# Optimization experiments

Hardware: AMD Instinct MI355X
Metric: run time of the kernel (lower is better)

The kernel has to match this reference:

```python
import jax, jax.numpy as jnp
import numpy as np

COMMITMENT_COST = 0.25
DECAY = 0.99
EPSILON = 1e-05


def setup_inputs() -> dict:
    key = jax.random.key(0)
    k1, k2, k3 = jax.random.split(key, 3)
    B, C, H, W = 64, 64, 64, 64  # C == embedding_dim
    K, D = 1024, 64
    return {
        "inputs": jax.random.normal(k1, (B, C, H, W), dtype=jnp.float32),
        "weight": jax.random.normal(k2, (K, D), dtype=jnp.float32),
        "ema_cluster_size": jnp.ones((K,), dtype=jnp.float32),
        "ema_w": jax.random.normal(k3, (K, D), dtype=jnp.float32),
    }


def reference(inputs, weight, ema_cluster_size, ema_w):
    K, D = weight.shape
    # NCHW -> NHWC, flatten to [N, D]
    x = jnp.transpose(inputs, (0, 2, 3, 1))
    flat = x.reshape(-1, D)
    # squared L2 distances to all codebook entries: [N, K]
    distances = (
        jnp.sum(flat * flat, axis=1, keepdims=True)
        + jnp.sum(weight * weight, axis=1)
        - 2.0 * flat @ weight.T
    )
    idx = jnp.argmin(distances, axis=1)  # [N]
    # training-mode EMA update (replaces the one-hot scatter + matmuls with segment sums)
    counts = jax.ops.segment_sum(jnp.ones_like(idx, dtype=flat.dtype), idx, num_segments=K)
    dw = jax.ops.segment_sum(flat, idx, num_segments=K)  # encodings.T @ flat_input
    cs = ema_cluster_size * DECAY + (1.0 - DECAY) * counts
    n = jnp.sum(cs)
    cs = (cs + EPSILON) / (n + K * EPSILON) * n  # Laplace smoothing
    ew = ema_w * DECAY + (1.0 - DECAY) * dw
    new_weight = ew / cs[:, None]
    # quantize with the UPDATED codebook (matches in-place torch order)
    quantized = new_weight[idx].reshape(x.shape)
    e_latent_loss = jnp.mean(jnp.square(jax.lax.stop_gradient(quantized) - x))
    loss = COMMITMENT_COST * e_latent_loss
    quantized_st = x + jax.lax.stop_gradient(quantized - x)  # straight-through
    return loss, jnp.transpose(quantized_st, (0, 3, 1, 2)), idx[:, None]
```

## Files before the change

kernel.cpp:

```cpp
#include <hip/hip_runtime.h>

#define K_CODES 1024
#define D_DIM   64
#define N_ROWS  262144
#define HW      4096
#define CHW     262144
#define N_ELEM  16777216
#define DECAY   0.99f
#define OMD     0.01f
#define EPS_F   1e-05f
#define MARGIN_BF 0.008f
#define FLAG_CAP 32768
#define SEG_CAP  2048
#define NHB      64
#define BROWS    128

typedef __attribute__((ext_vector_type(8))) short bf16x8;
typedef __attribute__((ext_vector_type(4))) float f32x4;

constexpr size_t OFF_LOSS    = 0;
constexpr size_t OFF_FLAGCNT = 8;
constexpr size_t OFF_DONE    = 12;
constexpr size_t ZERO_BYTES  = 64;
constexpr size_t OFF_W2F     = 64;
constexpr size_t OFF_W2D     = 4160;
constexpr size_t OFF_CS     = 12352;
constexpr size_t OFF_GOFF    = 16448;
constexpr size_t OFF_DW      = 20608;
constexpr size_t OFF_NEWW    = 282752;
constexpr size_t OFF_IDX     = 544896;
constexpr size_t OFF_HISTB   = 1593472;
constexpr size_t OFF_SORT    = 1855616;
constexpr size_t OFF_FLAGS   = 1855616;
constexpr size_t OFF_WFRAG   = 1986688;

__device__ __forceinline__ short f2bf(float f) {
    unsigned u = __float_as_uint(f);
    u += 0x7fffu + ((u >> 16) & 1u);
    return (short)(u >> 16);
}
__device__ __forceinline__ float bf2f(short h) {
    return __uint_as_float(((unsigned)(unsigned short)h) << 16);
}

__device__ __forceinline__ void gload_lds16(const float4* g, void* l) {
    __builtin_amdgcn_global_load_lds(
        (const __attribute__((address_space(1))) void*)g,
        (__attribute__((address_space(3))) void*)l, 16, 0, 0);
}

__global__ __launch_bounds__(256) void prep_kernel(
    const float* __restrict__ w, short* __restrict__ wfrag,
    float* __restrict__ w2f, double* __restrict__ w2d) {
    int t = threadIdx.x;
    if (blockIdx.x < 32) {
        int gid = blockIdx.x * 256 + t;
        int j = gid >> 7, h = (gid >> 6) & 1, L = gid & 63;
        int code = j * 16 + (L & 15);
        int kb = h * 32 + ((L >> 4) << 3);
        const float* wp = w + code * D_DIM + kb;
        short hi[8], lo[8];
#pragma unroll
        for (int i = 0; i < 8; ++i) {
            float v = wp[i];
            short hb = f2bf(v);
            hi[i] = hb;
            lo[i] = f2bf(v - bf2f(hb));
        }
        short* dh = wfrag + (size_t)(((j * 2 + h) * 2 + 0) * 64 + L) * 8;
        short* dl = wfrag + (size_t)(((j * 2 + h) * 2 + 1) * 64 + L) * 8;
#pragma unroll
        for (int i = 0; i < 8; ++i) { dh[i] = hi[i]; dl[i] = lo[i]; }
    } else {
        int k = (blockIdx.x - 32) * 256 + t;
        const float* wk = w + k * D_DIM;
        float sf = 0.f; double sd = 0.0;
#pragma unroll
        for (int d = 0; d < D_DIM; ++d) {
            float wv = wk[d];
            sf = fmaf(wv, wv, sf);
            sd = fma((double)wv, (double)wv, sd);
        }
        w2f[k] = sf; w2d[k] = sd;
    }
}

__global__ __launch_bounds__(256) __attribute__((amdgpu_waves_per_eu(2, 4)))
void argmin_kernel(
    const float* __restrict__ inp, const short* __restrict__ wfrag,
    const float* __restrict__ w2f, int* __restrict__ idx_ws,
    float* __restrict__ out_idx_f, float* __restrict__ xt,
    int* __restrict__ flagcnt, int* __restrict__ flaglist) {
    __shared__ float w2s[K_CODES];
    __shared__ alignas(16) char smem_u[64 * 68 * 4];
    __shared__ alignas(16) short bufA[8192];
    float (*xs)[68] = (float (*)[68])smem_u;
    short* bufB = (short*)smem_u;

    int t = threadIdx.x;
    ((float4*)w2s)[t] = ((const float4*)w2f)[t];

    int rowbase = blockIdx.x * BROWS;
    int b = rowbase >> 12, hwb = rowbase & (HW - 1);
    const float* xp = inp + (size_t)b * CHW + hwb;
    int lane = t & 63, wave = t >> 6;
    int q = lane >> 4, col = lane & 15;

    bf16x8 aH[2][2], aL[2][2];

    for (int p = 0; p < 2; ++p) {
#pragma unroll
        for (int it = 0; it < 16; ++it) {
            int d = wave * 16 + it;
            xs[lane][d] = xp[(size_t)d * HW + p * 64 + lane];
        }
        __syncthreads();

        float4* xt4 = (float4*)(xt + (size_t)(rowbase + p * 64) * D_DIM);
#pragma unroll
        for (int i2 = 0; i2 < 4; ++i2) {
            int c2 = t + i2 * 256;
            xt4[c2] = ((const float4*)xs[c2 >> 4])[c2 & 15];
        }

        if ((wave >> 1) == p) {
#pragma unroll
            for (int s2 = 0; s2 < 2; ++s2) {
                int rl = (wave & 1) * 32 + s2 * 16 + col;
#pragma unroll
                for (int h = 0; h < 2; ++h) {
#pragma unroll
                    for (int i = 0; i < 8; ++i) {
                        float v = xs[rl][h * 32 + q * 8 + i];
                        short hb = f2bf(v);
                        aH[s2][h][i] = hb;
                        aL[s2][h][i] = f2bf(v - bf2f(hb));
                    }
                }
            }
        }
        __syncthreads();
    }

    float best[2][4], best2[2][4];
#pragma unroll
    for (int s2 = 0; s2 < 2; ++s2)
#pragma unroll
        for (int r = 0; r < 4; ++r) { best[s2][r] = 3.4e38f; best2[s2][r] = 3.4e38f; }
    const float4* wsrc = (const float4*)wfrag;

    {
        const float4* src = wsrc + t;
        char* nb = (char*)bufA + wave * 1024;
#pragma unroll
        for (int i2 = 0; i2 < 4; ++i2)
            gload_lds16(src + i2 * 256, nb + i2 * 4096);
    }

    for (int st = 0; st < 16; ++st) {
        asm volatile("s_waitcnt vmcnt(0)" ::: "memory");
        __syncthreads();
        if (st < 15) {
            const float4* src = wsrc + (size_t)(st + 1) * 1024 + t;
            char* nb = ((st & 1) ? (char*)bufA : (char*)bufB) + wave * 1024;
#pragma unroll
            for (int i2 = 0; i2 < 4; ++i2)
                gload_lds16(src + i2 * 256, nb + i2 * 4096);
        }
        const bf16x8* wt = (const bf16x8*)((st & 1) ? bufB : bufA);

#pragma unroll
        for (int jj = 0; jj < 4; ++jj) {
            int j = st * 4 + jj;
            bf16x8 bh0 = wt[(jj * 4 + 0) * 64 + lane];
            bf16x8 bl0 = wt[(jj * 4 + 1) * 64 + lane];
            bf16x8 bh1 = wt[(jj * 4 + 2) * 64 + lane];
            bf16x8 bl1 = wt[(jj * 4 + 3) * 64 + lane];
            f32x4 acc0 = {0.f, 0.f, 0.f, 0.f};
            f32x4 acc1 = {0.f, 0.f, 0.f, 0.f};
            acc0 = __builtin_amdgcn_mfma_f32_16x16x32_bf16(aL[0][0], bh0, acc0, 0, 0, 0);
            acc1 = __builtin_amdgcn_mfma_f32_16x16x32_bf16(aL[1][0], bh0, acc1, 0, 0, 0);
            acc0 = __builtin_amdgcn_mfma_f32_16x16x32_bf16(aL[0][1], bh1, acc0, 0, 0, 0);
            acc1 = __builtin_amdgcn_mfma_f32_16x16x32_bf16(aL[1][1], bh1, acc1, 0, 0, 0);
            acc0 = __builtin_amdgcn_mfma_f32_16x16x32_bf16(aH[0][0], bl0, acc0, 0, 0, 0);
            acc1 = __builtin_amdgcn_mfma_f32_16x16x32_bf16(aH[1][0], bl0, acc1, 0, 0, 0);
            acc0 = __builtin_amdgcn_mfma_f32_16x16x32_bf16(aH[0][1], bl1, acc0, 0, 0, 0);
            acc1 = __builtin_amdgcn_mfma_f32_16x16x32_bf16(aH[1][1], bl1, acc1, 0, 0, 0);
            acc0 = __builtin_amdgcn_mfma_f32_16x16x32_bf16(aH[0][0], bh0, acc0, 0, 0, 0);
            acc1 = __builtin_amdgcn_mfma_f32_16x16x32_bf16(aH[1][0], bh0, acc1, 0, 0, 0);
            acc0 = __builtin_amdgcn_mfma_f32_16x16x32_bf16(aH[0][1], bh1, acc0, 0, 0, 0);
            acc1 = __builtin_amdgcn_mfma_f32_16x16x32_bf16(aH[1][1], bh1, acc1, 0, 0, 0);
            float w2c = w2s[j * 16 + col];
#pragma unroll
            for (int s2 = 0; s2 < 2; ++s2) {
#pragma unroll
                for (int r = 0; r < 4; ++r) {
                    float s = fmaf(-2.f, (s2 ? acc1 : acc0)[r], w2c);
                    float key = __int_as_float(
                        (__float_as_int(s) & ~63) | j);
                    best2[s2][r] = fminf(best2[s2][r], fmaxf(key, best[s2][r]));
                    best[s2][r]  = fminf(best[s2][r], key);
                }
            }
        }
    }

    int bk[2][4];
#pragma unroll
    for (int s2 = 0; s2 < 2; ++s2)
#pragma unroll
        for (int r = 0; r < 4; ++r)
            bk[s2][r] = ((__float_as_int(best[s2][r]) & 63) << 4) | col;

#pragma unroll
    for (int m = 1; m < 16; m <<= 1) {
#pragma unroll
        for (int s2 = 0; s2 < 2; ++s2) {
#pragma unroll
            for (int r = 0; r < 4; ++r) {
                float ob  = __shfl_xor(best[s2][r], m, 64);
                float ob2 = __shfl_xor(best2[s2][r], m, 64);
                int   obk = __shfl_xor(bk[s2][r], m, 64);
                float nb2 = fminf(fminf(best2[s2][r], ob2),
                                  fmaxf(best[s2][r], ob));
                int   nbk = ob < best[s2][r] ? obk
                            : (best[s2][r] < ob ? bk[s2][r]
                                                : min(bk[s2][r], obk));
                best[s2][r]  = fminf(best[s2][r], ob);
                best2[s2][r] = nb2;
                bk[s2][r]    = nbk;
            }
        }
    }

    if (col == 0) {
#pragma unroll
        for (int s2 = 0; s2 < 2; ++s2) {
#pragma unroll
            for (int r = 0; r < 4; ++r) {
                int row = rowbase + wave * 32 + s2 * 16 + q * 4 + r;
                idx_ws[row]    = bk[s2][r];
                out_idx_f[row] = (float)bk[s2][r];
                if (best2[s2][r] - best[s2][r] < MARGIN_BF) {
                    int pos = atomicAdd(flagcnt, 1);
                    if (pos < FLAG_CAP) flaglist[pos] = row;
                }
            }
        }
    }
}

__global__ __launch_bounds__(256) void refine_kernel(
    const float* __restrict__ xt, const float* __restrict__ weight,
    const double* __restrict__ w2d, int* __restrict__ idx_ws,
    float* __restrict__ out_idx_f, const int* __restrict__ flagcnt,
    const int* __restrict__ flaglist) {
    __shared__ float sx[4][64];
    int cnt = *flagcnt;
    if (cnt > FLAG_CAP) cnt = FLAG_CAP;
    int t = threadIdx.x, lane = t & 63, wave = t >> 6;

    for (int r = blockIdx.x * 4 + wave; r < cnt; r += gridDim.x * 4) {
        int row = flaglist[r];
        sx[wave][lane] = xt[(size_t)row * D_DIM + lane];
        asm volatile("s_waitcnt lgkmcnt(0)" ::: "memory");

        double bd = 1.0e300; int bi = 0;
        int k0 = lane * 16;
#pragma unroll 4
        for (int c = 0; c < 16; ++c) {
            int k = k0 + c;
            const float4* wk4 = (const float4*)(weight + (size_t)k * D_DIM);
            double dot = 0.0;
#pragma unroll
            for (int d4 = 0; d4 < 16; ++d4) {
                float4 wv = wk4[d4];
                dot = fma((double)wv.x, (double)sx[wave][d4 * 4 + 0], dot);
                dot = fma((double)wv.y, (double)sx[wave][d4 * 4 + 1], dot);
                dot = fma((double)wv.z, (double)sx[wave][d4 * 4 + 2], dot);
                dot = fma((double)wv.w, (double)sx[wave][d4 * 4 + 3], dot);
            }
            double dist = w2d[k] - 2.0 * dot;
            if (dist < bd) { bd = dist; bi = k; }
        }
#pragma unroll
        for (int m = 1; m < 64; m <<= 1) {
            double od = __shfl_xor(bd, m, 64);
            int    oi = __shfl_xor(bi, m, 64);
            if (od < bd || (od == bd && oi < bi)) { bd = od; bi = oi; }
        }
        if (lane == 0 && bi != idx_ws[row]) {
            idx_ws[row]    = bi;
            out_idx_f[row] = (float)bi;
        }
    }
}

__global__ __launch_bounds__(256) void hist_kernel(
    const int* __restrict__ idx_ws, int* __restrict__ histb) {
    __shared__ int h[K_CODES];
    int t = threadIdx.x, b = blockIdx.x;
    for (int i = t; i < K_CODES; i += 256) h[i] = 0;
    __syncthreads();
    const int4* idx4 = (const int4*)idx_ws + b * 1024;
#pragma unroll
    for (int i = 0; i < 4; ++i) {
        int4 c = idx4[t + i * 256];
        atomicAdd(&h[c.x], 1); atomicAdd(&h[c.y], 1);
        atomicAdd(&h[c.z], 1); atomicAdd(&h[c.w], 1);
    }
    __syncthreads();
    for (int i = t; i < K_CODES; i += 256) histb[b * K_CODES + i] = h[i];
}

__global__ __launch_bounds__(1024) void scan_kernel(
    int* __restrict__ histb, int* __restrict__ goff,
    const float* __restrict__ ema_cs, float* __restrict__ csbuf) {
    __shared__ int pre[K_CODES];
    __shared__ float red[K_CODES];
    int k = threadIdx.x;

    int s = 0;
    for (int b = 0; b < NHB; ++b) {
        int v = histb[b * K_CODES + k];
        histb[b * K_CODES + k] = s;
        s += v;
    }
    int cnt = s;

    pre[k] = cnt;
    __syncthreads();
    for (int d = 1; d < K_CODES; d <<= 1) {
        int v = (k >= d) ? pre[k - d] : 0;
        __syncthreads();
        if (k >= d) pre[k] += v;
        __syncthreads();
    }
    int base = pre[k] - cnt;
    goff[k] = base;
    if (k == K_CODES - 1) goff[K_CODES] = pre[k];

    for (int b = 0; b < NHB; ++b) histb[b * K_CODES + k] += base;

    float cs = ema_cs[k] * DECAY + OMD * (float)cnt;
    red[k] = cs;
    __syncthreads();
    for (int s2 = 512; s2 > 0; s2 >>= 1) {
        if (k < s2) red[k] += red[k + s2];
        __syncthreads();
    }
    float n = red[0];
    csbuf[k] = (cs + EPS_F) / (n + (float)K_CODES * EPS_F) * n;
}

__global__ __launch_bounds__(256) void scatter_kernel(
    const int* __restrict__ idx_ws, const int* __restrict__ histb,
    int* __restrict__ sorted) {
    __shared__ int cur[K_CODES];
    int t = threadIdx.x, b = blockIdx.x;
    for (int i = t; i < K_CODES; i += 256) cur[i] = histb[b * K_CODES + i];
    __syncthreads();
    const int4* idx4 = (const int4*)idx_ws + b * 1024;
#pragma unroll
    for (int i = 0; i < 4; ++i) {
        int4 c = idx4[t + i * 256];
        int r0 = (b * 1024 + t + i * 256) * 4;
        sorted[atomicAdd(&cur[c.x], 1)] = r0 + 0;
        sorted[atomicAdd(&cur[c.y], 1)] = r0 + 1;
        sorted[atomicAdd(&cur[c.z], 1)] = r0 + 2;
        sorted[atomicAdd(&cur[c.w], 1)] = r0 + 3;
    }
}

__global__ __launch_bounds__(256) void dwred_kernel(
    const float* __restrict__ xt, const int* __restrict__ sorted,
    const int* __restrict__ goff, const float* __restrict__ ema_w,
    const float* __restrict__ csbuf, float* __restrict__ new_w) {
    __shared__ int   rows[SEG_CAP];
    __shared__ float red[256];
    int k = blockIdx.x, t = threadIdx.x;
    int base = goff[k];
    int cnt = goff[k + 1] - base;
    int cc = cnt > SEG_CAP ? SEG_CAP : cnt;

    for (int i = t; i < cc; i += 256) rows[i] = sorted[base + i];
    __syncthreads();

    int d = t & 63, sub = t >> 6;
    float a0 = 0.f, a1 = 0.f;
    int i = sub;
    for (; i + 4 < cc; i += 8) {
        a0 += xt[(size_t)rows[i] * D_DIM + d];
        a1 += xt[(size_t)rows[i + 4] * D_DIM + d];
    }
    for (; i < cc; i += 4) a0 += xt[(size_t)rows[i] * D_DIM + d];
    red[t] = a0 + a1;
    __syncthreads();
    if (t < 64) {
        float dwv = red[t] + red[t + 64] + red[t + 128] + red[t + 192];
        new_w[k * D_DIM + t] =
            (ema_w[k * D_DIM + t] * DECAY + OMD * dwv) / csbuf[k];
    }
}

__global__ __launch_bounds__(256) void out_kernel(
    const float* __restrict__ inp, const float* __restrict__ new_w,
    const int* __restrict__ idx_ws, float* __restrict__ out,
    double* __restrict__ loss_acc, int* __restrict__ done_cnt) {
    int row = blockIdx.x * 256 + threadIdx.x;
    int b  = row >> 12;
    int hw = row & (HW - 1);
    const float* xp = inp + (size_t)b * CHW + hw;
    float* op = out + 1 + (size_t)b * CHW + hw;

    int k = idx_ws[row];
    const float* q = new_w + k * D_DIM;

    float lsum = 0.f;
#pragma unroll
    for (int d = 0; d < D_DIM; ++d) {
        float xv = xp[(size_t)d * HW];
        float qv = q[d];
        float diff = qv - xv;
        lsum = fmaf(diff, diff, lsum);
        op[(size_t)d * HW] = xv + diff;
    }

    __shared__ double lred[256];
    lred[threadIdx.x] = (double)lsum;
    __syncthreads();
    for (int s = 128; s > 0; s >>= 1) {
        if (threadIdx.x < s) lred[threadIdx.x] += lred[threadIdx.x + s];
        __syncthreads();
    }
    if (threadIdx.x == 0) {
        atomicAdd(loss_acc, lred[0]);
        __threadfence();
        int old = atomicAdd(done_cnt, 1);
        if (old == (int)gridDim.x - 1) {
            double v = atomicAdd(loss_acc, 0.0);
            out[0] = (float)(0.25 * (v / (double)N_ELEM));
        }
    }
}

extern "C" void kernel_launch(void* const* d_in, const int* in_sizes, int n_in,
                              void* d_out, int out_size, void* d_ws, size_t ws_size,
                              hipStream_t stream) {
    const float* inp    = (const float*)d_in[0];
    const float* weight = (const float*)d_in[1];
    const float* ema_cs = (const float*)d_in[2];
    const float* ema_w  = (const float*)d_in[3];
    float* out = (float*)d_out;

    char* ws = (char*)d_ws;
    double* loss_acc = (double*)(ws + OFF_LOSS);
    int*    flagcnt  = (int*)(ws + OFF_FLAGCNT);
    int*    done_cnt = (int*)(ws + OFF_DONE);
    float*  w2f      = (float*)(ws + OFF_W2F);
    double* w2d      = (double*)(ws + OFF_W2D);
    float*  csbuf    = (float*)(ws + OFF_CS);
    int*    goff     = (int*)(ws + OFF_GOFF);
    float*  new_w    = (float*)(ws + OFF_NEWW);
    int*    idx_ws   = (int*)(ws + OFF_IDX);
    int*    histb    = (int*)(ws + OFF_HISTB);
    int*    sorted   = (int*)(ws + OFF_SORT);
    int*    flaglist = (int*)(ws + OFF_FLAGS);
    short*  wfrag    = (short*)(ws + OFF_WFRAG);

    float* xt        = out + 1;
    float* out_idx_f = out + 1 + (size_t)N_ELEM;

    hipMemsetAsync(ws, 0, ZERO_BYTES, stream);

    prep_kernel<<<36, 256, 0, stream>>>(weight, wfrag, w2f, w2d);

    argmin_kernel<<<N_ROWS / BROWS, 256, 0, stream>>>(
        inp, wfrag, w2f, idx_ws, out_idx_f, xt, flagcnt, flaglist);

    refine_kernel<<<256, 256, 0, stream>>>(
        xt, weight, w2d, idx_ws, out_idx_f, flagcnt, flaglist);

    hist_kernel<<<NHB, 256, 0, stream>>>(idx_ws, histb);

    scan_kernel<<<1, 1024, 0, stream>>>(histb, goff, ema_cs, csbuf);

    scatter_kernel<<<NHB, 256, 0, stream>>>(idx_ws, histb, sorted);

    dwred_kernel<<<K_CODES, 256, 0, stream>>>(xt, sorted, goff, ema_w, csbuf, new_w);

    out_kernel<<<N_ROWS / 256, 256, 0, stream>>>(inp, new_w, idx_ws, out,
                                                 loss_acc, done_cnt);
}
```

Baseline: 436.1 us.

## Fold codebook norm into MFMA accumulator init and pair codes per iteration

The argmin kernel now seeds the MFMA accumulators with -0.5*||w||^2 and maximizes the dot-product score. This removes the per-element fma that scaled the result and added the norm, and the near-tie margin is halved to match the new scale. Two codes are processed per inner iteration so their MFMA chains interleave, and a top-2 merge runs on each pair. The memset is replaced by zeroing inside prep_kernel, and refine gets twice as many blocks. The risks are the extra register pressure from the paired accumulators and a near-tie flag test that now depends on the rescaled margin.

```diff
diff --git a/kernel.cpp b/kernel.cpp
--- a/kernel.cpp
+++ b/kernel.cpp
@@ -9,7 +9,7 @@
 #define DECAY   0.99f
 #define OMD     0.01f
 #define EPS_F   1e-05f
-#define MARGIN_BF 0.008f
+#define MARGIN_ACC 0.004f
 #define FLAG_CAP 32768
 #define SEG_CAP  2048
 #define NHB      64
@@ -21,12 +21,10 @@
 constexpr size_t OFF_LOSS    = 0;
 constexpr size_t OFF_FLAGCNT = 8;
 constexpr size_t OFF_DONE    = 12;
-constexpr size_t ZERO_BYTES  = 64;
 constexpr size_t OFF_W2F     = 64;
 constexpr size_t OFF_W2D     = 4160;
 constexpr size_t OFF_CS     = 12352;
 constexpr size_t OFF_GOFF    = 16448;
-constexpr size_t OFF_DW      = 20608;
 constexpr size_t OFF_NEWW    = 282752;
 constexpr size_t OFF_IDX     = 544896;
 constexpr size_t OFF_HISTB   = 1593472;
@@ -51,8 +49,10 @@
 
 __global__ __launch_bounds__(256) void prep_kernel(
     const float* __restrict__ w, short* __restrict__ wfrag,
-    float* __restrict__ w2f, double* __restrict__ w2d) {
+    float* __restrict__ w2f, double* __restrict__ w2d,
+    int* __restrict__ zero16) {
     int t = threadIdx.x;
+    if (blockIdx.x == 35 && t < 4) zero16[t] = 0;
     if (blockIdx.x < 32) {
         int gid = blockIdx.x * 256 + t;
         int j = gid >> 7, h = (gid >> 6) & 1, L = gid & 63;
@@ -146,7 +146,7 @@
 #pragma unroll
     for (int s2 = 0; s2 < 2; ++s2)
 #pragma unroll
-        for (int r = 0; r < 4; ++r) { best[s2][r] = 3.4e38f; best2[s2][r] = 3.4e38f; }
+        for (int r = 0; r < 4; ++r) { best[s2][r] = -3.4e38f; best2[s2][r] = -3.4e38f; }
     const float4* wsrc = (const float4*)wfrag;
 
     {
@@ -170,36 +170,58 @@
         const bf16x8* wt = (const bf16x8*)((st & 1) ? bufB : bufA);
 
 #pragma unroll
-        for (int jj = 0; jj < 4; ++jj) {
-            int j = st * 4 + jj;
-            bf16x8 bh0 = wt[(jj * 4 + 0) * 64 + lane];
-            bf16x8 bl0 = wt[(jj * 4 + 1) * 64 + lane];
-            bf16x8 bh1 = wt[(jj * 4 + 2) * 64 + lane];
-            bf16x8 bl1 = wt[(jj * 4 + 3) * 64 + lane];
-            f32x4 acc0 = {0.f, 0.f, 0.f, 0.f};
-            f32x4 acc1 = {0.f, 0.f, 0.f, 0.f};
-            acc0 = __builtin_amdgcn_mfma_f32_16x16x32_bf16(aL[0][0], bh0, acc0, 0, 0, 0);
-            acc1 = __builtin_amdgcn_mfma_f32_16x16x32_bf16(aL[1][0], bh0, acc1, 0, 0, 0);
-            acc0 = __builtin_amdgcn_mfma_f32_16x16x32_bf16(aL[0][1], bh1, acc0, 0, 0, 0);
-            acc1 = __builtin_amdgcn_mfma_f32_16x16x32_bf16(aL[1][1], bh1, acc1, 0, 0, 0);
-            acc0 = __builtin_amdgcn_mfma_f32_16x16x32_bf16(aH[0][0], bl0, acc0, 0, 0, 0);
-            acc1 = __builtin_amdgcn_mfma_f32_16x16x32_bf16(aH[1][0], bl0, acc1, 0, 0, 0);
-            acc0 = __builtin_amdgcn_mfma_f32_16x16x32_bf16(aH[0][1], bl1, acc0, 0, 0, 0);
-            acc1 = __builtin_amdgcn_mfma_f32_16x16x32_bf16(aH[1][1], bl1, acc1, 0, 0, 0);
-            acc0 = __builtin_amdgcn_mfma_f32_16x16x32_bf16(aH[0][0], bh0, acc0, 0, 0, 0);
-            acc1 = __builtin_amdgcn_mfma_f32_16x16x32_bf16(aH[1][0], bh0, acc1, 0, 0, 0);
-            acc0 = __builtin_amdgcn_mfma_f32_16x16x32_bf16(aH[0][1], bh1, acc0, 0, 0, 0);
-            acc1 = __builtin_amdgcn_mfma_f32_16x16x32_bf16(aH[1][1], bh1, acc1, 0, 0, 0);
-            float w2c = w2s[j * 16 + col];
+        for (int jp = 0; jp < 2; ++jp) {
+            int jA = st * 4 + jp * 2, jB = jA + 1;
+            int jjA = jp * 2, jjB = jp * 2 + 1;
+            bf16x8 bh0A = wt[(jjA * 4 + 0) * 64 + lane];
+            bf16x8 bl0A = wt[(jjA * 4 + 1) * 64 + lane];
+            bf16x8 bh1A = wt[(jjA * 4 + 2) * 64 + lane];
+            bf16x8 bl1A = wt[(jjA * 4 + 3) * 64 + lane];
+            bf16x8 bh0B = wt[(jjB * 4 + 0) * 64 + lane];
+            bf16x8 bl0B = wt[(jjB * 4 + 1) * 64 + lane];
+            bf16x8 bh1B = wt[(jjB * 4 + 2) * 64 + lane];
+            bf16x8 bl1B = wt[(jjB * 4 + 3) * 64 + lane];
+            float cA = -0.5f * w2s[jA * 16 + col];
+            float cB = -0.5f * w2s[jB * 16 + col];
+            f32x4 a0A = {cA, cA, cA, cA}, a1A = {cA, cA, cA, cA};
+            f32x4 a0B = {cB, cB, cB, cB}, a1B = {cB, cB, cB, cB};
+            a0A = __builtin_amdgcn_mfma_f32_16x16x32_bf16(aL[0][0], bh0A, a0A, 0, 0, 0);
+            a1A = __builtin_amdgcn_mfma_f32_16x16x32_bf16(aL[1][0], bh0A, a1A, 0, 0, 0);
+            a0B = __builtin_amdgcn_mfma_f32_16x16x32_bf16(aL[0][0], bh0B, a0B, 0, 0, 0);
+            a1B = __builtin_amdgcn_mfma_f32_16x16x32_bf16(aL[1][0], bh0B, a1B, 0, 0, 0);
+            a0A = __builtin_amdgcn_mfma_f32_16x16x32_bf16(aL[0][1], bh1A, a0A, 0, 0, 0);
+            a1A = __builtin_amdgcn_mfma_f32_16x16x32_bf16(aL[1][1], bh1A, a1A, 0, 0, 0);
+            a0B = __builtin_amdgcn_mfma_f32_16x16x32_bf16(aL[0][1], bh1B, a0B, 0, 0, 0);
+            a1B = __builtin_amdgcn_mfma_f32_16x16x32_bf16(aL[1][1], bh1B, a1B, 0, 0, 0);
+            a0A = __builtin_amdgcn_mfma_f32_16x16x32_bf16(aH[0][0], bl0A, a0A, 0, 0, 0);
+            a1A = __builtin_amdgcn_mfma_f32_16x16x32_bf16(aH[1][0], bl0A, a1A, 0, 0, 0);
+            a0B = __builtin_amdgcn_mfma_f32_16x16x32_bf16(aH[0][0], bl0B, a0B, 0, 0, 0);
+            a1B = __builtin_amdgcn_mfma_f32_16x16x32_bf16(aH[1][0], bl0B, a1B, 0, 0, 0);
+            a0A = __builtin_amdgcn_mfma_f32_16x16x32_bf16(aH[0][1], bl1A, a0A, 0, 0, 0);
+            a1A = __builtin_amdgcn_mfma_f32_16x16x32_bf16(aH[1][1], bl1A, a1A, 0, 0, 0);
+            a0B = __builtin_amdgcn_mfma_f32_16x16x32_bf16(aH[0][1], bl1B, a0B, 0, 0, 0);
+            a1B = __builtin_amdgcn_mfma_f32_16x16x32_bf16(aH[1][1], bl1B, a1B, 0, 0, 0);
+            a0A = __builtin_amdgcn_mfma_f32_16x16x32_bf16(aH[0][0], bh0A, a0A, 0, 0, 0);
+            a1A = __builtin_amdgcn_mfma_f32_16x16x32_bf16(aH[1][0], bh0A, a1A, 0, 0, 0);
+            a0B = __builtin_amdgcn_mfma_f32_16x16x32_bf16(aH[0][0], bh0B, a0B, 0, 0, 0);
+            a1B = __builtin_amdgcn_mfma_f32_16x16x32_bf16(aH[1][0], bh0B, a1B, 0, 0, 0);
+            a0A = __builtin_amdgcn_mfma_f32_16x16x32_bf16(aH[0][1], bh1A, a0A, 0, 0, 0);
+            a1A = __builtin_amdgcn_mfma_f32_16x16x32_bf16(aH[1][1], bh1A, a1A, 0, 0, 0);
+            a0B = __builtin_amdgcn_mfma_f32_16x16x32_bf16(aH[0][1], bh1B, a0B, 0, 0, 0);
+            a1B = __builtin_amdgcn_mfma_f32_16x16x32_bf16(aH[1][1], bh1B, a1B, 0, 0, 0);
 #pragma unroll
             for (int s2 = 0; s2 < 2; ++s2) {
 #pragma unroll
                 for (int r = 0; r < 4; ++r) {
-                    float s = fmaf(-2.f, (s2 ? acc1 : acc0)[r], w2c);
-                    float key = __int_as_float(
-                        (__float_as_int(s) & ~63) | j);
-                    best2[s2][r] = fminf(best2[s2][r], fmaxf(key, best[s2][r]));
-                    best[s2][r]  = fminf(best[s2][r], key);
+                    float vA = (s2 ? a1A : a0A)[r];
+                    float vB = (s2 ? a1B : a0B)[r];
+                    float kA = __int_as_float((__float_as_int(vA) & ~63) | jA);
+                    float kB = __int_as_float((__float_as_int(vB) & ~63) | jB);
+                    float hi = fmaxf(kA, kB);
+                    float lo = fminf(kA, kB);
+                    float tm = fminf(best[s2][r], hi);
+                    best2[s2][r] = fmaxf(fmaxf(tm, lo), best2[s2][r]);
+                    best[s2][r]  = fmaxf(best[s2][r], hi);
                 }
             }
         }
@@ -221,12 +243,12 @@
                 float ob  = __shfl_xor(best[s2][r], m, 64);
                 float ob2 = __shfl_xor(best2[s2][r], m, 64);
                 int   obk = __shfl_xor(bk[s2][r], m, 64);
-                float nb2 = fminf(fminf(best2[s2][r], ob2),
-                                  fmaxf(best[s2][r], ob));
-                int   nbk = ob < best[s2][r] ? obk
-                            : (best[s2][r] < ob ? bk[s2][r]
+                float nb2 = fmaxf(fmaxf(best2[s2][r], ob2),
+                                  fminf(best[s2][r], ob));
+                int   nbk = ob > best[s2][r] ? obk
+                            : (best[s2][r] > ob ? bk[s2][r]
                                                 : min(bk[s2][r], obk));
-                best[s2][r]  = fminf(best[s2][r], ob);
+                best[s2][r]  = fmaxf(best[s2][r], ob);
                 best2[s2][r] = nb2;
                 bk[s2][r]    = nbk;
             }
@@ -241,7 +263,7 @@
                 int row = rowbase + wave * 32 + s2 * 16 + q * 4 + r;
                 idx_ws[row]    = bk[s2][r];
                 out_idx_f[row] = (float)bk[s2][r];
-                if (best2[s2][r] - best[s2][r] < MARGIN_BF) {
+                if (best[s2][r] - best2[s2][r] < MARGIN_ACC) {
                     int pos = atomicAdd(flagcnt, 1);
                     if (pos < FLAG_CAP) flaglist[pos] = row;
                 }
@@ -471,14 +493,12 @@
     float* xt        = out + 1;
     float* out_idx_f = out + 1 + (size_t)N_ELEM;
 
-    hipMemsetAsync(ws, 0, ZERO_BYTES, stream);
-
-    prep_kernel<<<36, 256, 0, stream>>>(weight, wfrag, w2f, w2d);
+    prep_kernel<<<36, 256, 0, stream>>>(weight, wfrag, w2f, w2d, (int*)ws);
 
     argmin_kernel<<<N_ROWS / BROWS, 256, 0, stream>>>(
         inp, wfrag, w2f, idx_ws, out_idx_f, xt, flagcnt, flaglist);
 
-    refine_kernel<<<256, 256, 0, stream>>>(
+    refine_kernel<<<512, 256, 0, stream>>>(
         xt, weight, w2d, idx_ws, out_idx_f, flagcnt, flaglist);
 
     hist_kernel<<<NHB, 256, 0, stream>>>(idx_ws, histb);
```

After: 434.1 us. No clear change (-0.5%).
